# Optimization experiments

Hardware: AMD Instinct MI355X
Metric: run time of the kernel (lower is better)

The kernel has to match this reference:

```python
import jax, jax.numpy as jnp
import numpy as np

N, E, H, D, FE = 50000, 400000, 4, 64, 64  # nodes, edges, heads, per-head dim, edge feat dim
NEG_SLOPE = 0.2


def setup_inputs() -> dict:
    key = jax.random.key(0)
    ks = jax.random.split(key, 18)
    def p(k, shape, s=0.1):
        return jax.random.normal(k, shape, dtype=jnp.float32) * s
    return dict(
        features=p(ks[0], (N, D), 1.0),
        edge_feat=p(ks[1], (E, FE), 1.0),
        src=jax.random.randint(ks[2], (E,), 0, N),
        dst=jax.random.randint(ks[3], (E,), 0, N),
        # layer 0: in=64 -> H*D=256, residual Linear since 64 != 256
        W0=p(ks[4], (D, H * D)), We0=p(ks[5], (FE, H * D)),
        al0=p(ks[6], (H, D)), ar0=p(ks[7], (H, D)), ae0=p(ks[8], (H, D)),
        b0=p(ks[9], (H * D,)), Wres0=p(ks[10], (D, H * D)),
        # layer 1 (last): in=256 -> H*D=256, residual = identity view
        W1=p(ks[11], (H * D, H * D)), We1=p(ks[12], (FE, H * D)),
        al1=p(ks[13], (H, D)), ar1=p(ks[14], (H, D)), ae1=p(ks[15], (H, D)),
        b1=p(ks[16], (H * D,)),
    )


def _edge_gat_layer(h, ef, src, dst, W, We, al, ar, ae, b, Wres=None):
    n = h.shape[0]
    ft = (h @ W).reshape(n, H, D)          # (N,H,D) projected node feats
    fe = (ef @ We).reshape(-1, H, D)       # (E,H,D) projected edge feats
    el = jnp.sum(ft * al, axis=-1)         # (N,H)
    er = jnp.sum(ft * ar, axis=-1)         # (N,H)
    ee = jnp.sum(fe * ae, axis=-1)         # (E,H)
    e = el[src] + er[dst] + ee             # (E,H)
    e = jnp.where(e > 0, e, NEG_SLOPE * e)  # leaky_relu(0.2)
    # segment softmax over incoming edges of each dst node
    m = jax.ops.segment_max(jax.lax.stop_gradient(e), dst, num_segments=n)
    ex = jnp.exp(e - m[dst])
    den = jax.ops.segment_sum(ex, dst, num_segments=n)
    a = ex / den[dst]                      # (E,H) attention
    out = jax.ops.segment_sum(ft[src] * a[:, :, None], dst, num_segments=n)  # (N,H,D)
    res = (h @ Wres).reshape(n, H, D) if Wres is not None else h.reshape(n, H, D)
    return out + res + b.reshape(1, H, D)


def reference(features, edge_feat, src, dst,
              W0, We0, al0, ar0, ae0, b0, Wres0,
              W1, We1, al1, ar1, ae1, b1):
    h = _edge_gat_layer(features, edge_feat, src, dst, W0, We0, al0, ar0, ae0, b0, Wres0)
    h = jax.nn.elu(h.reshape(N, H * D))    # flatten heads + ELU between layers
    h = _edge_gat_layer(h, edge_feat, src, dst, W1, We1, al1, ar1, ae1, b1)
    return h.mean(axis=1)                  # (N, D) mean over heads on last layer
```

## Files before the change

### kernel.cpp

```cpp
#include <hip/hip_runtime.h>
#include <hip/hip_bf16.h>

#define NN 50000
#define EE 400000
#define NB 196

typedef __bf16 bf16_8 __attribute__((ext_vector_type(8)));
typedef float f32x4 __attribute__((ext_vector_type(4)));

__global__ __launch_bounds__(256) void prep_kernel(
    const float* __restrict__ features, __bf16* __restrict__ fbf,
    const float* __restrict__ W0, const float* __restrict__ Wres0, __bf16* __restrict__ Bt0,
    const float* __restrict__ W1, __bf16* __restrict__ Bt1,
    const float* __restrict__ We0, const float* __restrict__ ae0, float* __restrict__ Ve0,
    const float* __restrict__ We1, const float* __restrict__ ae1, float* __restrict__ Ve1,
    const int* __restrict__ dst, int* __restrict__ cnt) {
  int b = blockIdx.x;
  int t = threadIdx.x;
  if (b < 1563) {
    int i = b * 256 + t;
    if (i < NN * 64 / 8) {
      const float4* p = (const float4*)features + (size_t)i * 2;
      float4 a = p[0], c = p[1];
      bf16_8 v = {(__bf16)a.x, (__bf16)a.y, (__bf16)a.z, (__bf16)a.w,
                  (__bf16)c.x, (__bf16)c.y, (__bf16)c.z, (__bf16)c.w};
      *(bf16_8*)(fbf + (size_t)i * 8) = v;
    }
  } else if (b < 1563 + 128) {
    int idx = (b - 1563) * 256 + t;
    int j = idx >> 6, k = idx & 63;
    float v = (j < 256) ? W0[k * 256 + j] : Wres0[k * 256 + (j - 256)];
    Bt0[idx] = (__bf16)v;
  } else if (b < 1563 + 128 + 256) {
    int idx = (b - 1563 - 128) * 256 + t;
    int j = idx >> 8, k = idx & 255;
    Bt1[idx] = (__bf16)W1[k * 256 + j];
  } else if (b == 1947) {
    int f = t >> 2, h = t & 3;
    float s = 0.f;
    for (int d = 0; d < 64; ++d) s += We0[f * 256 + h * 64 + d] * ae0[h * 64 + d];
    Ve0[f * 4 + h] = s;
  } else if (b == 1948) {
    int f = t >> 2, h = t & 3;
    float s = 0.f;
    for (int d = 0; d < 64; ++d) s += We1[f * 256 + h * 64 + d] * ae1[h * 64 + d];
    Ve1[f * 4 + h] = s;
  } else {
    int e = (b - 1949) * 256 + t;
    if (e < EE) atomicAdd(&cnt[dst[e]], 1);
  }
}

__global__ __launch_bounds__(256) void scan1_kernel(const int* __restrict__ cnt,
                                                    int* __restrict__ scanbuf,
                                                    int* __restrict__ blocksum) {
  __shared__ int s[256];
  int t = threadIdx.x;
  int idx = blockIdx.x * 256 + t;
  int c = (idx < NN) ? cnt[idx] : 0;
  s[t] = c;
  __syncthreads();
  for (int d = 1; d < 256; d <<= 1) {
    int v = (t >= d) ? s[t - d] : 0;
    __syncthreads();
    s[t] += v;
    __syncthreads();
  }
  if (idx < NN) scanbuf[idx] = s[t];
  if (t == 255) blocksum[blockIdx.x] = s[255];
}

__global__ __launch_bounds__(256) void scan2_kernel(const int* __restrict__ blocksum,
                                                    int* __restrict__ blockoff, int nb) {
  __shared__ int s[256];
  int t = threadIdx.x;
  int c = (t < nb) ? blocksum[t] : 0;
  s[t] = c;
  __syncthreads();
  for (int d = 1; d < 256; d <<= 1) {
    int v = (t >= d) ? s[t - d] : 0;
    __syncthreads();
    s[t] += v;
    __syncthreads();
  }
  if (t < nb) blockoff[t] = s[t] - c;
}

__global__ __launch_bounds__(256) void scan3_kernel(const int* __restrict__ scanbuf,
                                                    const int* __restrict__ cnt,
                                                    const int* __restrict__ blockoff,
                                                    int* __restrict__ off,
                                                    int* __restrict__ cur) {
  int idx = blockIdx.x * 256 + threadIdx.x;
  if (idx < NN) {
    int o = blockoff[blockIdx.x] + scanbuf[idx] - cnt[idx];
    off[idx] = o;
    cur[idx] = o;
  }
  if (idx == 0) off[NN] = EE;
}

__global__ __launch_bounds__(256) void fill_kernel(const int* __restrict__ src,
                                                   const int* __restrict__ dst,
                                                   int* __restrict__ cur,
                                                   int* __restrict__ srcc,
                                                   int* __restrict__ eidc) {
  int e = blockIdx.x * 256 + threadIdx.x;
  if (e < EE) {
    int p = atomicAdd(&cur[dst[e]], 1);
    srcc[p] = src[e];
    eidc[p] = e;
  }
}

__global__ __launch_bounds__(256) void eek_kernel(const float* __restrict__ ef,
                                                  const float* __restrict__ Ve0,
                                                  const float* __restrict__ Ve1,
                                                  float* __restrict__ eeo) {
  __shared__ float V0[256], V1[256];
  V0[threadIdx.x] = Ve0[threadIdx.x];
  V1[threadIdx.x] = Ve1[threadIdx.x];
  __syncthreads();
  int r = threadIdx.x >> 2, sub = threadIdx.x & 3;
  int e = blockIdx.x * 64 + r;
  if (e >= EE) return;
  float a0 = 0, a1 = 0, a2 = 0, a3 = 0;
  float c0 = 0, c1 = 0, c2 = 0, c3 = 0;
  const float* row = ef + (size_t)e * 64 + sub * 16;
#pragma unroll
  for (int i = 0; i < 16; i += 4) {
    float4 v = *(const float4*)(row + i);
    float xs[4] = {v.x, v.y, v.z, v.w};
#pragma unroll
    for (int j = 0; j < 4; ++j) {
      float x = xs[j];
      int idx = (sub * 16 + i + j) * 4;
      a0 += x * V0[idx + 0]; a1 += x * V0[idx + 1];
      a2 += x * V0[idx + 2]; a3 += x * V0[idx + 3];
      c0 += x * V1[idx + 0]; c1 += x * V1[idx + 1];
      c2 += x * V1[idx + 2]; c3 += x * V1[idx + 3];
    }
  }
#pragma unroll
  for (int o = 1; o < 4; o <<= 1) {
    a0 += __shfl_xor(a0, o); a1 += __shfl_xor(a1, o);
    a2 += __shfl_xor(a2, o); a3 += __shfl_xor(a3, o);
    c0 += __shfl_xor(c0, o); c1 += __shfl_xor(c1, o);
    c2 += __shfl_xor(c2, o); c3 += __shfl_xor(c3, o);
  }
  if (sub == 0) {
    float4 u; u.x = a0; u.y = a1; u.z = a2; u.w = a3;
    float4 w; w.x = c0; w.y = c1; w.z = c2; w.w = c3;
    *(float4*)(eeo + (size_t)e * 8) = u;
    *(float4*)(eeo + (size_t)e * 8 + 4) = w;
  }
}

#define LDK 40
__global__ __launch_bounds__(256) void gemm_kernel(const __bf16* __restrict__ A,
                                                   const __bf16* __restrict__ Bt,
                                                   __bf16* __restrict__ ft,
                                                   __bf16* __restrict__ base,
                                                   const float* __restrict__ bias,
                                                   const float* __restrict__ al,
                                                   const float* __restrict__ ar,
                                                   float* __restrict__ el,
                                                   float* __restrict__ er,
                                                   int M, int K) {
  __shared__ __align__(16) __bf16 Al[64 * LDK];
  __shared__ __align__(16) __bf16 Bl[64 * LDK];
  int tid = threadIdx.x;
  int wav = tid >> 6, lane = tid & 63;
  int quad = lane >> 4, l16 = lane & 15;
  int bm = blockIdx.x * 64;
  int bn = blockIdx.y * 64;
  int sr = tid >> 2;
  int sk = (tid & 3) << 3;

  f32x4 acc[4] = {{0, 0, 0, 0}, {0, 0, 0, 0}, {0, 0, 0, 0}, {0, 0, 0, 0}};

  for (int k0 = 0; k0 < K; k0 += 32) {
    uint4 av = {0, 0, 0, 0};
    int arow = bm + sr;
    if (arow < M) av = *(const uint4*)(A + (size_t)arow * K + k0 + sk);
    uint4 bv = *(const uint4*)(Bt + (size_t)(bn + sr) * K + k0 + sk);
    __syncthreads();
    *(uint4*)&Al[sr * LDK + sk] = av;
    *(uint4*)&Bl[sr * LDK + sk] = bv;
    __syncthreads();
    bf16_8 af = *(const bf16_8*)&Al[(wav * 16 + l16) * LDK + quad * 8];
#pragma unroll
    for (int nt = 0; nt < 4; ++nt) {
      bf16_8 bf = *(const bf16_8*)&Bl[(nt * 16 + l16) * LDK + quad * 8];
      acc[nt] = __builtin_amdgcn_mfma_f32_16x16x32_bf16(af, bf, acc[nt], 0, 0, 0);
    }
  }

  int row0 = bm + wav * 16 + quad * 4;

  if (bn < 256) {
    int hb = bn >> 6;
#pragma unroll
    for (int r = 0; r < 4; ++r) {
      float pl = 0.f, pr = 0.f;
#pragma unroll
      for (int nt = 0; nt < 4; ++nt) {
        float v = acc[nt][r];
        int d = nt * 16 + l16;
        pl += v * al[hb * 64 + d];
        pr += v * ar[hb * 64 + d];
      }
#pragma unroll
      for (int o2 = 8; o2 > 0; o2 >>= 1) {
        pl += __shfl_xor(pl, o2);
        pr += __shfl_xor(pr, o2);
      }
      int row = row0 + r;
      if (l16 == 0 && row < M) {
        el[row * 4 + hb] = pl;
        er[row * 4 + hb] = pr;
      }
    }
  }

#pragma unroll
  for (int nt = 0; nt < 4; ++nt) {
    int col = bn + nt * 16 + l16;
#pragma unroll
    for (int r = 0; r < 4; ++r) {
      int row = row0 + r;
      if (row < M) {
        float v = acc[nt][r];
        if (col < 256)
          ft[(size_t)row * 256 + col] = (__bf16)v;
        else
          base[(size_t)row * 256 + (col - 256)] = (__bf16)(v + bias[col - 256]);
      }
    }
  }
}

template <int LAYER>
__global__ __launch_bounds__(256) void agg_kernel(const int* __restrict__ off,
                                                  const int* __restrict__ srcc,
                                                  const int* __restrict__ eidc,
                                                  const float* __restrict__ eeo,
                                                  const float* __restrict__ el,
                                                  const float* __restrict__ er,
                                                  const __bf16* __restrict__ ft,
                                                  const __bf16* prev,
                                                  const float* __restrict__ bias,
                                                  __bf16* outb,
                                                  float* __restrict__ outf) {
  __shared__ float red[256];
  int n = blockIdx.x;
  int t = threadIdx.x, h = t >> 6, lane = t & 63;
  int beg = off[n], end = off[n + 1];
  float pv = (float)prev[(size_t)n * 256 + t];
  float bv = (LAYER == 1) ? bias[t] : 0.f;
  float ern = er[n * 4 + h];
  int offd = h * 64 + lane;

  float acc = 0.f, den = 0.f;
  int j = beg;
  for (; j + 4 <= end; j += 4) {
    int s0 = srcc[j], s1 = srcc[j + 1], s2 = srcc[j + 2], s3 = srcc[j + 3];
    int e0 = eidc[j], e1 = eidc[j + 1], e2 = eidc[j + 2], e3 = eidc[j + 3];
    float z0 = el[s0 * 4 + h] + ern + eeo[(size_t)e0 * 8 + LAYER * 4 + h];
    float z1 = el[s1 * 4 + h] + ern + eeo[(size_t)e1 * 8 + LAYER * 4 + h];
    float z2 = el[s2 * 4 + h] + ern + eeo[(size_t)e2 * 8 + LAYER * 4 + h];
    float z3 = el[s3 * 4 + h] + ern + eeo[(size_t)e3 * 8 + LAYER * 4 + h];
    float w0 = __expf(z0 > 0.f ? z0 : 0.2f * z0);
    float w1 = __expf(z1 > 0.f ? z1 : 0.2f * z1);
    float w2 = __expf(z2 > 0.f ? z2 : 0.2f * z2);
    float w3 = __expf(z3 > 0.f ? z3 : 0.2f * z3);
    float v0 = (float)ft[(size_t)s0 * 256 + offd];
    float v1 = (float)ft[(size_t)s1 * 256 + offd];
    float v2 = (float)ft[(size_t)s2 * 256 + offd];
    float v3 = (float)ft[(size_t)s3 * 256 + offd];
    acc += w0 * v0; acc += w1 * v1; acc += w2 * v2; acc += w3 * v3;
    den += w0 + w1 + w2 + w3;
  }
  for (; j < end; ++j) {
    int s = srcc[j];
    float z = el[s * 4 + h] + ern + eeo[(size_t)eidc[j] * 8 + LAYER * 4 + h];
    float w = __expf(z > 0.f ? z : 0.2f * z);
    acc += w * (float)ft[(size_t)s * 256 + offd];
    den += w;
  }
  float res = (end > beg) ? acc / den : 0.f;

  if (LAYER == 0) {
    float v = res + pv;
    v = v > 0.f ? v : (__expf(v) - 1.0f);
    outb[(size_t)n * 256 + t] = (__bf16)v;
  } else {
    red[t] = res + pv + bv;
    __syncthreads();
    if (t < 64)
      outf[(size_t)n * 64 + t] =
          0.25f * (red[t] + red[t + 64] + red[t + 128] + red[t + 192]);
  }
}

extern "C" void kernel_launch(void* const* d_in, const int* in_sizes, int n_in,
                              void* d_out, int out_size, void* d_ws, size_t ws_size,
                              hipStream_t stream) {
  const float* features  = (const float*)d_in[0];
  const float* edge_feat = (const float*)d_in[1];
  const int*   src       = (const int*)d_in[2];
  const int*   dst       = (const int*)d_in[3];
  const float* W0    = (const float*)d_in[4];
  const float* We0   = (const float*)d_in[5];
  const float* al0   = (const float*)d_in[6];
  const float* ar0   = (const float*)d_in[7];
  const float* ae0   = (const float*)d_in[8];
  const float* b0    = (const float*)d_in[9];
  const float* Wres0 = (const float*)d_in[10];
  const float* W1    = (const float*)d_in[11];
  const float* We1   = (const float*)d_in[12];
  const float* al1   = (const float*)d_in[13];
  const float* ar1   = (const float*)d_in[14];
  const float* ae1   = (const float*)d_in[15];
  const float* b1    = (const float*)d_in[16];
  float* out = (float*)d_out;

  char* ws = (char*)d_ws;
  size_t o = 0;
  auto alloc = [&](size_t bytes) {
    void* p = ws + o;
    o = (o + bytes + 255) & ~(size_t)255;
    return p;
  };
  int*    cnt      = (int*)alloc((size_t)NN * 4);
  int*    scanbuf  = (int*)alloc((size_t)NN * 4);
  int*    blocksum = (int*)alloc(256 * 4);
  int*    blockoff = (int*)alloc(256 * 4);
  int*    off      = (int*)alloc((size_t)(NN + 1) * 4);
  int*    cur      = (int*)alloc((size_t)NN * 4);
  int*    srcc     = (int*)alloc((size_t)EE * 4);
  int*    eidc     = (int*)alloc((size_t)EE * 4);
  float*  eeo      = (float*)alloc((size_t)EE * 8 * 4);
  float*  el       = (float*)alloc((size_t)NN * 4 * 4);
  float*  er       = (float*)alloc((size_t)NN * 4 * 4);
  float*  Ve0      = (float*)alloc(256 * 4);
  float*  Ve1      = (float*)alloc(256 * 4);
  __bf16* Bt0      = (__bf16*)alloc((size_t)512 * 64 * 2);
  __bf16* Bt1      = (__bf16*)alloc((size_t)256 * 256 * 2);
  __bf16* fbf      = (__bf16*)alloc((size_t)NN * 64 * 2);
  __bf16* ft       = (__bf16*)alloc((size_t)NN * 256 * 2);
  __bf16* base     = (__bf16*)alloc((size_t)NN * 256 * 2);
  __bf16* h1       = base;

  const int EB = (EE + 255) / 256;
  const int MG = (NN + 63) / 64;

  hipMemsetAsync(cnt, 0, (size_t)NN * 4, stream);
  prep_kernel<<<1949 + EB, 256, 0, stream>>>(features, fbf, W0, Wres0, Bt0, W1, Bt1,
                                             We0, ae0, Ve0, We1, ae1, Ve1, dst, cnt);
  scan1_kernel<<<NB, 256, 0, stream>>>(cnt, scanbuf, blocksum);
  scan2_kernel<<<1, 256, 0, stream>>>(blocksum, blockoff, NB);
  scan3_kernel<<<NB, 256, 0, stream>>>(scanbuf, cnt, blockoff, off, cur);
  fill_kernel<<<EB, 256, 0, stream>>>(src, dst, cur, srcc, eidc);
  eek_kernel<<<(EE + 63) / 64, 256, 0, stream>>>(edge_feat, Ve0, Ve1, eeo);

  gemm_kernel<<<dim3(MG, 8), 256, 0, stream>>>(fbf, Bt0, ft, base, b0, al0, ar0, el, er, NN, 64);
  agg_kernel<0><<<NN, 256, 0, stream>>>(off, srcc, eidc, eeo, el, er, ft, base, nullptr, h1, nullptr);

  gemm_kernel<<<dim3(MG, 4), 256, 0, stream>>>(h1, Bt1, ft, nullptr, nullptr, al1, ar1, el, er, NN, 256);
  agg_kernel<1><<<NN, 256, 0, stream>>>(off, srcc, eidc, eeo, el, er, ft, h1, b1, nullptr, out);
}
```

Baseline: 444.8 us.

## Precompute per-edge attention weights in CSR order and broadcast via readlane

A new per-edge kernel computes the exp(leaky_relu) attention weights for all four heads once per layer and scatters them into CSR order. Before, each of the 64 lanes of a head computed these weights redundantly. The aggregation kernel now loads 64 source indices and weights cooperatively, one per lane, and broadcasts them with readlane. This removes the dependent loads of eid, el and eeo from the inner loop. In exchange it adds two extra edge passes with scattered writes and an extra edge-sized buffer.

Result: no change. 436.5 us (-1.9%).

```diff
diff --git a/kernel.cpp b/kernel.cpp
--- a/kernel.cpp
+++ b/kernel.cpp
@@ -104,19 +104,20 @@
                                                    const int* __restrict__ dst,
                                                    int* __restrict__ cur,
                                                    int* __restrict__ srcc,
-                                                   int* __restrict__ eidc) {
+                                                   int* __restrict__ pose) {
   int e = blockIdx.x * 256 + threadIdx.x;
   if (e < EE) {
     int p = atomicAdd(&cur[dst[e]], 1);
     srcc[p] = src[e];
-    eidc[p] = e;
+    pose[e] = p;
   }
 }
 
 __global__ __launch_bounds__(256) void eek_kernel(const float* __restrict__ ef,
                                                   const float* __restrict__ Ve0,
                                                   const float* __restrict__ Ve1,
-                                                  float* __restrict__ eeo) {
+                                                  float* __restrict__ eeo0,
+                                                  float* __restrict__ eeo1) {
   __shared__ float V0[256], V1[256];
   V0[threadIdx.x] = Ve0[threadIdx.x];
   V1[threadIdx.x] = Ve1[threadIdx.x];
@@ -151,8 +152,8 @@
   if (sub == 0) {
     float4 u; u.x = a0; u.y = a1; u.z = a2; u.w = a3;
     float4 w; w.x = c0; w.y = c1; w.z = c2; w.w = c3;
-    *(float4*)(eeo + (size_t)e * 8) = u;
-    *(float4*)(eeo + (size_t)e * 8 + 4) = w;
+    *(float4*)(eeo0 + (size_t)e * 4) = u;
+    *(float4*)(eeo1 + (size_t)e * 4) = w;
   }
 }
 
@@ -240,13 +241,32 @@
   }
 }
 
+__global__ __launch_bounds__(256) void wk_kernel(const int* __restrict__ src,
+                                                 const int* __restrict__ dst,
+                                                 const int* __restrict__ pose,
+                                                 const float* __restrict__ ee,
+                                                 const float* __restrict__ el,
+                                                 const float* __restrict__ er,
+                                                 float* __restrict__ wcsr) {
+  int e = blockIdx.x * 256 + threadIdx.x;
+  if (e >= EE) return;
+  int s = src[e], d = dst[e], p = pose[e];
+  float4 z4 = *(const float4*)(ee + (size_t)e * 4);
+  float4 e_l = *(const float4*)(el + (size_t)s * 4);
+  float4 e_r = *(const float4*)(er + (size_t)d * 4);
+  float4 w;
+  float z;
+  z = e_l.x + e_r.x + z4.x; w.x = __expf(z > 0.f ? z : 0.2f * z);
+  z = e_l.y + e_r.y + z4.y; w.y = __expf(z > 0.f ? z : 0.2f * z);
+  z = e_l.z + e_r.z + z4.z; w.z = __expf(z > 0.f ? z : 0.2f * z);
+  z = e_l.w + e_r.w + z4.w; w.w = __expf(z > 0.f ? z : 0.2f * z);
+  *(float4*)(wcsr + (size_t)p * 4) = w;
+}
+
 template <int LAYER>
 __global__ __launch_bounds__(256) void agg_kernel(const int* __restrict__ off,
                                                   const int* __restrict__ srcc,
-                                                  const int* __restrict__ eidc,
-                                                  const float* __restrict__ eeo,
-                                                  const float* __restrict__ el,
-                                                  const float* __restrict__ er,
+                                                  const float* __restrict__ wcsr,
                                                   const __bf16* __restrict__ ft,
                                                   const __bf16* prev,
                                                   const float* __restrict__ bias,
@@ -258,35 +278,41 @@
   int beg = off[n], end = off[n + 1];
   float pv = (float)prev[(size_t)n * 256 + t];
   float bv = (LAYER == 1) ? bias[t] : 0.f;
-  float ern = er[n * 4 + h];
   int offd = h * 64 + lane;
 
   float acc = 0.f, den = 0.f;
-  int j = beg;
-  for (; j + 4 <= end; j += 4) {
-    int s0 = srcc[j], s1 = srcc[j + 1], s2 = srcc[j + 2], s3 = srcc[j + 3];
-    int e0 = eidc[j], e1 = eidc[j + 1], e2 = eidc[j + 2], e3 = eidc[j + 3];
-    float z0 = el[s0 * 4 + h] + ern + eeo[(size_t)e0 * 8 + LAYER * 4 + h];
-    float z1 = el[s1 * 4 + h] + ern + eeo[(size_t)e1 * 8 + LAYER * 4 + h];
-    float z2 = el[s2 * 4 + h] + ern + eeo[(size_t)e2 * 8 + LAYER * 4 + h];
-    float z3 = el[s3 * 4 + h] + ern + eeo[(size_t)e3 * 8 + LAYER * 4 + h];
-    float w0 = __expf(z0 > 0.f ? z0 : 0.2f * z0);
-    float w1 = __expf(z1 > 0.f ? z1 : 0.2f * z1);
-    float w2 = __expf(z2 > 0.f ? z2 : 0.2f * z2);
-    float w3 = __expf(z3 > 0.f ? z3 : 0.2f * z3);
-    float v0 = (float)ft[(size_t)s0 * 256 + offd];
-    float v1 = (float)ft[(size_t)s1 * 256 + offd];
-    float v2 = (float)ft[(size_t)s2 * 256 + offd];
-    float v3 = (float)ft[(size_t)s3 * 256 + offd];
-    acc += w0 * v0; acc += w1 * v1; acc += w2 * v2; acc += w3 * v3;
-    den += w0 + w1 + w2 + w3;
-  }
-  for (; j < end; ++j) {
-    int s = srcc[j];
-    float z = el[s * 4 + h] + ern + eeo[(size_t)eidc[j] * 8 + LAYER * 4 + h];
-    float w = __expf(z > 0.f ? z : 0.2f * z);
-    acc += w * (float)ft[(size_t)s * 256 + offd];
-    den += w;
+  for (int c = beg; c < end; c += 64) {
+    int rem = end - c;
+    if (rem > 64) rem = 64;
+    int sv = 0;
+    float wv = 0.f;
+    if (lane < rem) {
+      sv = srcc[c + lane];
+      wv = wcsr[(size_t)(c + lane) * 4 + h];
+    }
+    int k = 0;
+    for (; k + 4 <= rem; k += 4) {
+      int s0 = __builtin_amdgcn_readlane(sv, k);
+      int s1 = __builtin_amdgcn_readlane(sv, k + 1);
+      int s2 = __builtin_amdgcn_readlane(sv, k + 2);
+      int s3 = __builtin_amdgcn_readlane(sv, k + 3);
+      float w0 = __uint_as_float(__builtin_amdgcn_readlane(__float_as_uint(wv), k));
+      float w1 = __uint_as_float(__builtin_amdgcn_readlane(__float_as_uint(wv), k + 1));
+      float w2 = __uint_as_float(__builtin_amdgcn_readlane(__float_as_uint(wv), k + 2));
+      float w3 = __uint_as_float(__builtin_amdgcn_readlane(__float_as_uint(wv), k + 3));
+      float v0 = (float)ft[(size_t)s0 * 256 + offd];
+      float v1 = (float)ft[(size_t)s1 * 256 + offd];
+      float v2 = (float)ft[(size_t)s2 * 256 + offd];
+      float v3 = (float)ft[(size_t)s3 * 256 + offd];
+      acc += w0 * v0; acc += w1 * v1; acc += w2 * v2; acc += w3 * v3;
+      den += w0 + w1 + w2 + w3;
+    }
+    for (; k < rem; ++k) {
+      int s = __builtin_amdgcn_readlane(sv, k);
+      float w = __uint_as_float(__builtin_amdgcn_readlane(__float_as_uint(wv), k));
+      acc += w * (float)ft[(size_t)s * 256 + offd];
+      den += w;
+    }
   }
   float res = (end > beg) ? acc / den : 0.f;
 
@@ -339,8 +365,10 @@
   int*    off      = (int*)alloc((size_t)(NN + 1) * 4);
   int*    cur      = (int*)alloc((size_t)NN * 4);
   int*    srcc     = (int*)alloc((size_t)EE * 4);
-  int*    eidc     = (int*)alloc((size_t)EE * 4);
-  float*  eeo      = (float*)alloc((size_t)EE * 8 * 4);
+  int*    pose     = (int*)alloc((size_t)EE * 4);
+  float*  eeo0     = (float*)alloc((size_t)EE * 4 * 4);
+  float*  eeo1     = (float*)alloc((size_t)EE * 4 * 4);
+  float*  wcsr     = (float*)alloc((size_t)EE * 4 * 4);
   float*  el       = (float*)alloc((size_t)NN * 4 * 4);
   float*  er       = (float*)alloc((size_t)NN * 4 * 4);
   float*  Ve0      = (float*)alloc(256 * 4);
@@ -361,12 +389,14 @@
   scan1_kernel<<<NB, 256, 0, stream>>>(cnt, scanbuf, blocksum);
   scan2_kernel<<<1, 256, 0, stream>>>(blocksum, blockoff, NB);
   scan3_kernel<<<NB, 256, 0, stream>>>(scanbuf, cnt, blockoff, off, cur);
-  fill_kernel<<<EB, 256, 0, stream>>>(src, dst, cur, srcc, eidc);
-  eek_kernel<<<(EE + 63) / 64, 256, 0, stream>>>(edge_feat, Ve0, Ve1, eeo);
+  fill_kernel<<<EB, 256, 0, stream>>>(src, dst, cur, srcc, pose);
+  eek_kernel<<<(EE + 63) / 64, 256, 0, stream>>>(edge_feat, Ve0, Ve1, eeo0, eeo1);
 
   gemm_kernel<<<dim3(MG, 8), 256, 0, stream>>>(fbf, Bt0, ft, base, b0, al0, ar0, el, er, NN, 64);
-  agg_kernel<0><<<NN, 256, 0, stream>>>(off, srcc, eidc, eeo, el, er, ft, base, nullptr, h1, nullptr);
+  wk_kernel<<<EB, 256, 0, stream>>>(src, dst, pose, eeo0, el, er, wcsr);
+  agg_kernel<0><<<NN, 256, 0, stream>>>(off, srcc, wcsr, ft, base, nullptr, h1, nullptr);
 
   gemm_kernel<<<dim3(MG, 4), 256, 0, stream>>>(h1, Bt1, ft, nullptr, nullptr, al1, ar1, el, er, NN, 256);
-  agg_kernel<1><<<NN, 256, 0, stream>>>(off, srcc, eidc, eeo, el, er, ft, h1, b1, nullptr, out);
-}
+  wk_kernel<<<EB, 256, 0, stream>>>(src, dst, pose, eeo1, el, er, wcsr);
+  agg_kernel<1><<<NN, 256, 0, stream>>>(off, srcc, wcsr, ft, h1, b1, nullptr, out);
+}
```
